# Kernel optimization log

Hardware: AMD Instinct MI355X
Metric: run time of the kernel (lower is better)

Reference implementation:

```python
import jax, jax.numpy as jnp
import numpy as np

B, H, HF = 2048, 128, 10  # batch, bi-LSTM hidden, fc-LSTM hidden


def _lstm(x_seq, h0, c0, Wih, Whh, bih, bhh):
    """Unidirectional LSTM, PyTorch gate order (i, f, g, o).
    x_seq: [T, B, I]. Returns final (h, c), each [B, H].
    Input projection is hoisted out of the scan (one big GEMM)."""
    pre = jnp.einsum('tbi,gi->tbg', x_seq, Wih) + bih + bhh  # [T, B, 4H]

    def step(carry, p):
        h, c = carry
        g = p + h @ Whh.T
        i, f, gg, o = jnp.split(g, 4, axis=-1)
        c = jax.nn.sigmoid(f) * c + jax.nn.sigmoid(i) * jnp.tanh(gg)
        h = jax.nn.sigmoid(o) * jnp.tanh(c)
        return (h, c), None

    (hT, cT), _ = jax.lax.scan(step, (h0, c0), pre)
    return hT, cT


def setup_inputs() -> dict:
    key = jax.random.key(0)
    ks = iter(jax.random.split(key, 40))
    s = 1.0 / np.sqrt(H)
    sf = 1.0 / np.sqrt(HF)
    u = lambda shape, sc: jax.random.uniform(next(ks), shape, jnp.float32, -sc, sc)
    inp = {"x": jax.random.normal(next(ks), (B, 28, 28), jnp.float32)}
    for name in ["lr_f", "lr_b", "ud_f", "ud_b"]:
        inp["Wih_" + name] = u((4 * H, 28), s)
        inp["Whh_" + name] = u((4 * H, H), s)
        inp["bih_" + name] = u((4 * H,), s)
        inp["bhh_" + name] = u((4 * H,), s)
    inp["Wih_fc"] = u((4 * HF, 1), sf)
    inp["Whh_fc"] = u((4 * HF, HF), sf)
    inp["bih_fc"] = u((4 * HF,), sf)
    inp["bhh_fc"] = u((4 * HF,), sf)
    for name in ["h0_lr", "c0_lr", "h0_ud", "c0_ud"]:
        inp[name] = jax.random.normal(next(ks), (2, B, H), jnp.float32)
    inp["h0_fc"] = jax.random.normal(next(ks), (B, HF), jnp.float32)
    inp["c0_fc"] = jax.random.normal(next(ks), (B, HF), jnp.float32)
    return inp


def reference(x, Wih_lr_f, Whh_lr_f, bih_lr_f, bhh_lr_f,
              Wih_lr_b, Whh_lr_b, bih_lr_b, bhh_lr_b,
              Wih_ud_f, Whh_ud_f, bih_ud_f, bhh_ud_f,
              Wih_ud_b, Whh_ud_b, bih_ud_b, bhh_ud_b,
              Wih_fc, Whh_fc, bih_fc, bhh_fc,
              h0_lr, c0_lr, h0_ud, c0_ud, h0_fc, c0_fc):
    x_lr = jnp.transpose(x, (1, 0, 2))  # [28, B, 28]: rows as time
    x_ud = jnp.transpose(x, (2, 0, 1))  # [28, B, 28]: cols as time
    # bidirectional = forward scan + scan over reversed sequence
    h_lr_f, _ = _lstm(x_lr, h0_lr[0], c0_lr[0], Wih_lr_f, Whh_lr_f, bih_lr_f, bhh_lr_f)
    h_lr_b, _ = _lstm(x_lr[::-1], h0_lr[1], c0_lr[1], Wih_lr_b, Whh_lr_b, bih_lr_b, bhh_lr_b)
    h_ud_f, _ = _lstm(x_ud, h0_ud[0], c0_ud[0], Wih_ud_f, Whh_ud_f, bih_ud_f, bhh_ud_f)
    h_ud_b, _ = _lstm(x_ud[::-1], h0_ud[1], c0_ud[1], Wih_ud_b, Whh_ud_b, bih_ud_b, bhh_ud_b)
    feat = jnp.concatenate([h_lr_f, h_lr_b, h_ud_f, h_ud_b], axis=1)  # [B, 4H]
    seq = feat.T[:, :, None]  # [4H, B, 1]: feature index is the fc-LSTM time axis
    h_f, _ = _lstm(seq, h0_fc, c0_fc, Wih_fc, Whh_fc, bih_fc, bhh_fc)  # [B, 10]
    return jax.nn.log_softmax(h_f, axis=1)
```

## Files before the change

kernel.cpp:

```cpp
#include <hip/hip_runtime.h>
#include <hip/hip_bf16.h>

typedef __bf16   bf16x8 __attribute__((ext_vector_type(8)));
typedef float    f32x4  __attribute__((ext_vector_type(4)));
typedef _Float16 h16x2  __attribute__((ext_vector_type(2)));

#define LOG2E 1.4426950408889634f
#define LN2   0.6931471805599453f

__device__ __forceinline__ float rcp_(float x){
#if __has_builtin(__builtin_amdgcn_rcpf)
  return __builtin_amdgcn_rcpf(x);
#else
  return 1.0f / x;
#endif
}
__device__ __forceinline__ float ex2_(float x){
#if __has_builtin(__builtin_amdgcn_exp2f)
  return __builtin_amdgcn_exp2f(x);
#else
  return exp2f(x);
#endif
}
__device__ __forceinline__ float lg2_(float x){
#if __has_builtin(__builtin_amdgcn_logf)
  return __builtin_amdgcn_logf(x);
#else
  return log2f(x);
#endif
}

__device__ __forceinline__ int pkrtz_(float a, float b){
  auto v = __builtin_amdgcn_cvt_pkrtz(a, b);
  int r; __builtin_memcpy(&r, &v, 4); return r;
}
__device__ __forceinline__ h16x2 as_h2_(int x){
  h16x2 r; __builtin_memcpy(&r, &x, 4); return r;
}

#if __has_builtin(__builtin_amdgcn_fdot2)
__device__ __forceinline__ float fdot2_(int w, int h, float a){
  return __builtin_amdgcn_fdot2(as_h2_(w), as_h2_(h), a, false);
}
#else
__device__ __forceinline__ float fdot2_(int w, int h, float a){
  h16x2 wv = as_h2_(w), hv = as_h2_(h);
  return a + (float)wv[0]*(float)hv[0] + (float)wv[1]*(float)hv[1];
}
#endif

struct LstmArgs {
  const float* Wih[4]; const float* Whh[4];
  const float* bih[4]; const float* bhh[4];
  const float* h0[4];  const float* c0[4];
};

__global__ void pack_weights(LstmArgs args, bf16x8* __restrict__ wpack,
                             float* __restrict__ bpack)
{
  const int idx = blockIdx.x*256 + threadIdx.x;
  if (idx >= 4*8*4*5*64) return;
  const int lane = idx & 63;
  int r = idx >> 6;
  const int kk = r % 5; r /= 5;
  const int g  = r & 3; r >>= 2;
  const int w  = r & 7;
  const int d  = r >> 3;
  const int lc = lane & 15, lr4 = lane >> 4;
  const int grow = g*128 + w*16 + lc;
  const float sc = (g == 2) ? 2.0f*LOG2E : -LOG2E;

  bf16x8 v;
  if (kk < 4){
    const float* p = args.Whh[d] + grow*128 + kk*32 + lr4*8;
#pragma unroll
    for (int j = 0; j < 8; ++j) v[j] = (__bf16)(p[j] * sc);
  } else {
#pragma unroll
    for (int j = 0; j < 8; ++j){
      const int xi = lr4*8 + j;
      v[j] = (xi < 28) ? (__bf16)(args.Wih[d][grow*28 + xi] * sc) : (__bf16)0.0f;
    }
  }
  wpack[idx] = v;
  if (kk == 0 && lr4 == 0)
    bpack[d*512 + grow] = (args.bih[d][grow] + args.bhh[d][grow]) * sc;
}

__global__ __launch_bounds__(512, 2) void lstm4_kernel(const float* __restrict__ x,
                                                       LstmArgs args,
                                                       const bf16x8* __restrict__ wpack,
                                                       const float* __restrict__ bpack,
                                                       __bf16* __restrict__ featB)
{
  const int dir = blockIdx.x >> 6;
  const int b0  = (blockIdx.x & 63) * 32;
  const int tid = threadIdx.x;
  const int w   = tid >> 6;
  const int l   = tid & 63;
  const int lc  = l & 15;
  const int lr4 = l >> 4;

  const float* __restrict__ h0 = args.h0[dir];
  const float* __restrict__ c0 = args.c0[dir];
  const int rev = dir & 1;
  const bool lrdir = (dir < 2);

  __shared__ __align__(16) __bf16 hcat[2][32 * 168];
  __shared__ __align__(16) __bf16 xstage[28 * 32 * 40];

  bf16x8 bfr[4][5];
  f32x4  bias_acc[4];
  {
    const bf16x8* wp = wpack + (dir*8 + w)*4*5*64;
#pragma unroll
    for (int g = 0; g < 4; ++g){
#pragma unroll
      for (int kk = 0; kk < 5; ++kk)
        bfr[g][kk] = wp[(g*5 + kk)*64 + l];
      const float b = bpack[dir*512 + g*128 + w*16 + lc];
      f32x4 bv = {b, b, b, b};
      bias_acc[g] = bv;
    }
  }

  for (int idx = tid; idx < 32*196; idx += 512){
    const int row = idx / 196;
    const int rem = idx - row*196;
    if (lrdir){
      const int t = rem / 7, jg = rem - 7*t;
      const float4 v = *(const float4*)&x[(b0+row)*784 + t*28 + jg*4];
      __bf16* dst = &xstage[(t*32 + row)*40 + jg*4];
      dst[0]=(__bf16)v.x; dst[1]=(__bf16)v.y; dst[2]=(__bf16)v.z; dst[3]=(__bf16)v.w;
    } else {
      const int j = rem / 7, tg = rem - 7*j;
      const float4 v = *(const float4*)&x[(b0+row)*784 + j*28 + tg*4];
      xstage[((tg*4+0)*32 + row)*40 + j] = (__bf16)v.x;
      xstage[((tg*4+1)*32 + row)*40 + j] = (__bf16)v.y;
      xstage[((tg*4+2)*32 + row)*40 + j] = (__bf16)v.z;
      xstage[((tg*4+3)*32 + row)*40 + j] = (__bf16)v.w;
    }
  }
  for (int idx = tid; idx < 28*32; idx += 512){
    const int t = idx >> 5, row = idx & 31;
    __bf16* p = &xstage[(t*32 + row)*40 + 28];
    p[0] = p[1] = p[2] = p[3] = (__bf16)0.0f;
  }

  float cst[2][4];
#pragma unroll
  for (int m = 0; m < 2; ++m)
#pragma unroll
  for (int r = 0; r < 4; ++r){
    const int row = 16*m + 4*lr4 + r;
    const int col = w*16 + lc;
    cst[m][r] = c0[(b0+row)*128 + col];
    hcat[0][row*168 + col] = (__bf16)h0[(b0+row)*128 + col];
  }
  __syncthreads();

  int cur = 0;
  for (int s = 0; s < 28; ++s){
    const int t = rev ? (27 - s) : s;
    const int nxt = cur ^ 1;

    f32x4 acc[2][4];
#pragma unroll
    for (int m = 0; m < 2; ++m){
#pragma unroll
      for (int kk = 0; kk < 5; ++kk){
        const bf16x8 a = (kk < 4)
          ? *(const bf16x8*)&hcat[cur][(16*m + lc)*168 + kk*32 + lr4*8]
          : *(const bf16x8*)&xstage[(t*32 + 16*m + lc)*40 + lr4*8];
        if (kk == 0){
#pragma unroll
          for (int g = 0; g < 4; ++g)
            acc[m][g] = __builtin_amdgcn_mfma_f32_16x16x32_bf16(a, bfr[g][0], bias_acc[g], 0, 0, 0);
        } else {
#pragma unroll
          for (int g = 0; g < 4; ++g)
            acc[m][g] = __builtin_amdgcn_mfma_f32_16x16x32_bf16(a, bfr[g][kk], acc[m][g], 0, 0, 0);
        }
      }
    }

#pragma unroll
    for (int m = 0; m < 2; ++m)
#pragma unroll
    for (int r = 0; r < 4; ++r){
      const float Ei = ex2_(acc[m][0][r]);
      const float Ef = ex2_(acc[m][1][r]);
      const float Eg = ex2_(acc[m][2][r]);
      const float Eo = ex2_(acc[m][3][r]);
      const float u  = 1.0f + Ei;
      const float v  = 1.0f + Eg;
      const float wf = 1.0f + Ef;
      const float P  = u * v;
      const float R  = rcp_(P * wf);
      const float num = __builtin_fmaf(cst[m][r], P, (v - 2.0f) * wf);
      const float cc  = num * R;
      cst[m][r] = cc;
      const float Ec  = ex2_(2.0f*LOG2E*cc);
      const float roc = rcp_((1.0f + Eo)*(1.0f + Ec));
      const float hv  = (Ec - 1.0f)*roc;
      hcat[nxt][(16*m + 4*lr4 + r)*168 + w*16 + lc] = (__bf16)hv;
    }
    __syncthreads();
    cur = nxt;
  }

  {
    const int row = tid >> 4;
    const int cg  = tid & 15;
    const bf16x8 hv = *(const bf16x8*)&hcat[cur][row*168 + cg*8];
    *(bf16x8*)&featB[(b0+row)*512 + dir*128 + cg*8] = hv;
  }
}

__global__ __launch_bounds__(256) void fc_lstm_wave(const ushort* __restrict__ featB,
                                                    const float* __restrict__ Wih,
                                                    const float* __restrict__ Whh,
                                                    const float* __restrict__ bih,
                                                    const float* __restrict__ bhh,
                                                    const float* __restrict__ h0,
                                                    const float* __restrict__ c0,
                                                    float* __restrict__ out)
{
  const int tid = threadIdx.x;
  const int l   = tid & 63;
  const int e   = blockIdx.x*4 + (tid >> 6);
  const int u   = l >> 2;
  const int g   = l & 3;
  const int uc  = (u < 10) ? u : 9;
  const bool valid = (u < 10);
  const float sc = (g == 2) ? 2.0f*LOG2E : -LOG2E;
  const int row = g*10 + uc;

  int wh2[5];
#pragma unroll
  for (int m = 0; m < 5; ++m){
    const float w0 = valid ? Whh[row*10 + 2*m]   * sc : 0.0f;
    const float w1 = valid ? Whh[row*10 + 2*m+1] * sc : 0.0f;
    wh2[m] = pkrtz_(w0, w1);
  }
  const float wx   = valid ? Wih[row]*sc : 0.0f;
  const float bia  = valid ? (bih[row] + bhh[row])*sc : 0.0f;
  const float actA = (g == 2) ? 1.0f : 0.0f;
  const float actB = (g == 2) ? -2.0f : 1.0f;

  float c     = valid ? c0[e*10 + uc] : 0.0f;
  float hlast = valid ? h0[e*10 + uc] : 0.0f;

  int hp0, hp1, hp2, hp3, hp4;
  {
    const int hn = __builtin_amdgcn_mov_dpp(__float_as_int(hlast), 0x104, 0xF, 0xF, false);
    const int hpi = pkrtz_(hlast, __int_as_float(hn));
    hp0 = __builtin_amdgcn_readlane(hpi,  0);
    hp1 = __builtin_amdgcn_readlane(hpi,  8);
    hp2 = __builtin_amdgcn_readlane(hpi, 16);
    hp3 = __builtin_amdgcn_readlane(hpi, 24);
    hp4 = __builtin_amdgcn_readlane(hpi, 32);
  }

  const uint4* fBs;
  {
    unsigned long long a = (unsigned long long)(uintptr_t)(featB + (size_t)e*512);
    unsigned lo = (unsigned)__builtin_amdgcn_readfirstlane((int)(a & 0xffffffffu));
    unsigned hi = (unsigned)__builtin_amdgcn_readfirstlane((int)(a >> 32));
    fBs = (const uint4*)(uintptr_t)(((unsigned long long)hi << 32) | lo);
  }

  unsigned int cur[8][4], nxt[8][4];
#pragma unroll
  for (int k = 0; k < 8; ++k){
    const uint4 q0 = fBs[k];
    cur[k][0]=q0.x; cur[k][1]=q0.y; cur[k][2]=q0.z; cur[k][3]=q0.w;
    const uint4 q1 = fBs[8 + k];
    nxt[k][0]=q1.x; nxt[k][1]=q1.y; nxt[k][2]=q1.z; nxt[k][3]=q1.w;
  }

  for (int win = 0; win < 8; ++win){
#pragma unroll
    for (int blk = 0; blk < 8; ++blk){
#pragma unroll
      for (int jj = 0; jj < 8; ++jj){
        const unsigned d  = cur[blk][jj >> 1];
        const unsigned xb = (jj & 1) ? (d & 0xffff0000u) : (d << 16);
        const float xs = __int_as_float((int)xb);
        float a0 = __builtin_fmaf(wx, xs, bia);
        a0 = fdot2_(wh2[0], hp0, a0);
        float a1 = fdot2_(wh2[1], hp1, 0.0f);
        a0 = fdot2_(wh2[2], hp2, a0);
        a1 = fdot2_(wh2[3], hp3, a1);
        a0 = fdot2_(wh2[4], hp4, a0);
        const float acc = a0 + a1;
        const float rc  = rcp_(1.0f + ex2_(acc));
        const float val = __builtin_fmaf(actB, rc, actA);
        const int   vi  = __float_as_int(val);
        const float tg  = __int_as_float(__builtin_amdgcn_mov_dpp(vi, 0xAA, 0xF, 0xF, false));
        const float sf  = __int_as_float(__builtin_amdgcn_mov_dpp(vi, 0x55, 0xF, 0xF, false));
        const float so  = __int_as_float(__builtin_amdgcn_mov_dpp(vi, 0xFF, 0xF, 0xF, false));
        c = __builtin_fmaf(sf, c, val*tg);
        const float tc = __builtin_fmaf(-2.0f, rcp_(1.0f + ex2_(2.0f*LOG2E*c)), 1.0f);
        const float h  = so*tc;
        hlast = h;
        const int hn  = __builtin_amdgcn_mov_dpp(__float_as_int(h), 0x104, 0xF, 0xF, false);
        const int hpi = pkrtz_(h, __int_as_float(hn));
        hp0 = __builtin_amdgcn_readlane(hpi,  0);
        hp1 = __builtin_amdgcn_readlane(hpi,  8);
        hp2 = __builtin_amdgcn_readlane(hpi, 16);
        hp3 = __builtin_amdgcn_readlane(hpi, 24);
        hp4 = __builtin_amdgcn_readlane(hpi, 32);
      }
    }
#pragma unroll
    for (int k = 0; k < 8; ++k){
      cur[k][0]=nxt[k][0]; cur[k][1]=nxt[k][1];
      cur[k][2]=nxt[k][2]; cur[k][3]=nxt[k][3];
    }
    if (win < 6){
#pragma unroll
      for (int k = 0; k < 8; ++k){
        const uint4 q = fBs[(win + 2)*8 + k];
        nxt[k][0]=q.x; nxt[k][1]=q.y; nxt[k][2]=q.z; nxt[k][3]=q.w;
      }
    }
  }

  const int hb = __float_as_int(hlast);
  float sh[10];
#pragma unroll
  for (int m = 0; m < 10; ++m)
    sh[m] = __int_as_float(__builtin_amdgcn_readlane(hb, 4*m));
  float mx = sh[0];
#pragma unroll
  for (int m = 1; m < 10; ++m) mx = fmaxf(mx, sh[m]);
  float es = 0.0f;
#pragma unroll
  for (int m = 0; m < 10; ++m) es += ex2_(LOG2E*(sh[m] - mx));
  const float lse = LN2 * lg2_(es);
  if (valid && g == 0) out[e*10 + u] = hlast - mx - lse;
}

extern "C" void kernel_launch(void* const* d_in, const int* in_sizes, int n_in,
                              void* d_out, int out_size, void* d_ws, size_t ws_size,
                              hipStream_t stream)
{
  const float* x = (const float*)d_in[0];
  LstmArgs a;
  const int base[4] = {1, 5, 9, 13};
  for (int d = 0; d < 4; ++d){
    a.Wih[d] = (const float*)d_in[base[d] + 0];
    a.Whh[d] = (const float*)d_in[base[d] + 1];
    a.bih[d] = (const float*)d_in[base[d] + 2];
    a.bhh[d] = (const float*)d_in[base[d] + 3];
  }
  const float* h0lr = (const float*)d_in[21];
  const float* c0lr = (const float*)d_in[22];
  const float* h0ud = (const float*)d_in[23];
  const float* c0ud = (const float*)d_in[24];
  a.h0[0] = h0lr;               a.c0[0] = c0lr;
  a.h0[1] = h0lr + 2048*128;    a.c0[1] = c0lr + 2048*128;
  a.h0[2] = h0ud;               a.c0[2] = c0ud;
  a.h0[3] = h0ud + 2048*128;    a.c0[3] = c0ud + 2048*128;

  char* ws = (char*)d_ws;
  __bf16* featB = (__bf16*)ws;
  bf16x8* wpack = (bf16x8*)(ws + (2u<<20));
  float*  bpack = (float*)(ws + (2u<<20) + 655360u);

  pack_weights<<<160, 256, 0, stream>>>(a, wpack, bpack);
  lstm4_kernel<<<256, 512, 0, stream>>>(x, a, wpack, bpack, featB);
  fc_lstm_wave<<<512, 256, 0, stream>>>((const ushort*)featB,
      (const float*)d_in[17], (const float*)d_in[18],
      (const float*)d_in[19], (const float*)d_in[20],
      (const float*)d_in[25], (const float*)d_in[26],
      (float*)d_out);
}
```

Measured before the change: 126.4 us.

## Halve batch tile per LSTM block and fold bias into input MFMA column

Each block of the bidirectional LSTM kernel now handles 16 batch rows instead of 32, which doubles the grid to 512 blocks and raises the launch-bounds occupancy hint to 4 blocks per CU. The gate bias is folded into the padded input weight column, multiplied by a constant 1.0 written into the staged input. This removes the separate bias buffer and the bias accumulator registers. The aim is more parallelism across CUs on the latency-bound 28-step recurrence. In exchange each wave issues half as many MFMAs per step, and the bias is now rounded to bf16.

```diff
diff --git a/kernel.cpp b/kernel.cpp
--- a/kernel.cpp
+++ b/kernel.cpp
@@ -55,8 +55,7 @@
   const float* h0[4];  const float* c0[4];
 };
 
-__global__ void pack_weights(LstmArgs args, bf16x8* __restrict__ wpack,
-                             float* __restrict__ bpack)
+__global__ void pack_weights(LstmArgs args, bf16x8* __restrict__ wpack)
 {
   const int idx = blockIdx.x*256 + threadIdx.x;
   if (idx >= 4*8*4*5*64) return;
@@ -79,22 +78,23 @@
 #pragma unroll
     for (int j = 0; j < 8; ++j){
       const int xi = lr4*8 + j;
-      v[j] = (xi < 28) ? (__bf16)(args.Wih[d][grow*28 + xi] * sc) : (__bf16)0.0f;
+      float wv;
+      if (xi < 28)       wv = args.Wih[d][grow*28 + xi] * sc;
+      else if (xi == 28) wv = (args.bih[d][grow] + args.bhh[d][grow]) * sc;
+      else               wv = 0.0f;
+      v[j] = (__bf16)wv;
     }
   }
   wpack[idx] = v;
-  if (kk == 0 && lr4 == 0)
-    bpack[d*512 + grow] = (args.bih[d][grow] + args.bhh[d][grow]) * sc;
-}
-
-__global__ __launch_bounds__(512, 2) void lstm4_kernel(const float* __restrict__ x,
+}
+
+__global__ __launch_bounds__(512, 4) void lstm4_kernel(const float* __restrict__ x,
                                                        LstmArgs args,
                                                        const bf16x8* __restrict__ wpack,
-                                                       const float* __restrict__ bpack,
                                                        __bf16* __restrict__ featB)
 {
-  const int dir = blockIdx.x >> 6;
-  const int b0  = (blockIdx.x & 63) * 32;
+  const int dir = blockIdx.x >> 7;
+  const int b0  = (blockIdx.x & 127) * 16;
   const int tid = threadIdx.x;
   const int w   = tid >> 6;
   const int l   = tid & 63;
@@ -106,110 +106,100 @@
   const int rev = dir & 1;
   const bool lrdir = (dir < 2);
 
-  __shared__ __align__(16) __bf16 hcat[2][32 * 168];
-  __shared__ __align__(16) __bf16 xstage[28 * 32 * 40];
+  __shared__ __align__(16) __bf16 hcat[2][16 * 168];
+  __shared__ __align__(16) __bf16 xstage[28 * 16 * 40];
 
   bf16x8 bfr[4][5];
-  f32x4  bias_acc[4];
   {
     const bf16x8* wp = wpack + (dir*8 + w)*4*5*64;
 #pragma unroll
-    for (int g = 0; g < 4; ++g){
+    for (int g = 0; g < 4; ++g)
 #pragma unroll
       for (int kk = 0; kk < 5; ++kk)
         bfr[g][kk] = wp[(g*5 + kk)*64 + l];
-      const float b = bpack[dir*512 + g*128 + w*16 + lc];
-      f32x4 bv = {b, b, b, b};
-      bias_acc[g] = bv;
-    }
-  }
-
-  for (int idx = tid; idx < 32*196; idx += 512){
+  }
+
+  for (int idx = tid; idx < 16*196; idx += 512){
     const int row = idx / 196;
     const int rem = idx - row*196;
     if (lrdir){
       const int t = rem / 7, jg = rem - 7*t;
       const float4 v = *(const float4*)&x[(b0+row)*784 + t*28 + jg*4];
-      __bf16* dst = &xstage[(t*32 + row)*40 + jg*4];
+      __bf16* dst = &xstage[(t*16 + row)*40 + jg*4];
       dst[0]=(__bf16)v.x; dst[1]=(__bf16)v.y; dst[2]=(__bf16)v.z; dst[3]=(__bf16)v.w;
     } else {
       const int j = rem / 7, tg = rem - 7*j;
       const float4 v = *(const float4*)&x[(b0+row)*784 + j*28 + tg*4];
-      xstage[((tg*4+0)*32 + row)*40 + j] = (__bf16)v.x;
-      xstage[((tg*4+1)*32 + row)*40 + j] = (__bf16)v.y;
-      xstage[((tg*4+2)*32 + row)*40 + j] = (__bf16)v.z;
-      xstage[((tg*4+3)*32 + row)*40 + j] = (__bf16)v.w;
-    }
-  }
-  for (int idx = tid; idx < 28*32; idx += 512){
-    const int t = idx >> 5, row = idx & 31;
-    __bf16* p = &xstage[(t*32 + row)*40 + 28];
-    p[0] = p[1] = p[2] = p[3] = (__bf16)0.0f;
-  }
-
-  float cst[2][4];
-#pragma unroll
-  for (int m = 0; m < 2; ++m)
+      xstage[((tg*4+0)*16 + row)*40 + j] = (__bf16)v.x;
+      xstage[((tg*4+1)*16 + row)*40 + j] = (__bf16)v.y;
+      xstage[((tg*4+2)*16 + row)*40 + j] = (__bf16)v.z;
+      xstage[((tg*4+3)*16 + row)*40 + j] = (__bf16)v.w;
+    }
+  }
+  if (tid < 28*16){
+    const int t = tid >> 4, row = tid & 15;
+    __bf16* p = &xstage[(t*16 + row)*40 + 28];
+    p[0] = (__bf16)1.0f; p[1] = (__bf16)0.0f; p[2] = (__bf16)0.0f; p[3] = (__bf16)0.0f;
+  }
+
+  float cst[4];
 #pragma unroll
   for (int r = 0; r < 4; ++r){
-    const int row = 16*m + 4*lr4 + r;
+    const int row = 4*lr4 + r;
     const int col = w*16 + lc;
-    cst[m][r] = c0[(b0+row)*128 + col];
+    cst[r] = c0[(b0+row)*128 + col];
     hcat[0][row*168 + col] = (__bf16)h0[(b0+row)*128 + col];
   }
   __syncthreads();
+
+  const f32x4 zacc = {0.0f, 0.0f, 0.0f, 0.0f};
 
   int cur = 0;
   for (int s = 0; s < 28; ++s){
     const int t = rev ? (27 - s) : s;
     const int nxt = cur ^ 1;
 
-    f32x4 acc[2][4];
-#pragma unroll
-    for (int m = 0; m < 2; ++m){
-#pragma unroll
-      for (int kk = 0; kk < 5; ++kk){
-        const bf16x8 a = (kk < 4)
-          ? *(const bf16x8*)&hcat[cur][(16*m + lc)*168 + kk*32 + lr4*8]
-          : *(const bf16x8*)&xstage[(t*32 + 16*m + lc)*40 + lr4*8];
-        if (kk == 0){
-#pragma unroll
-          for (int g = 0; g < 4; ++g)
-            acc[m][g] = __builtin_amdgcn_mfma_f32_16x16x32_bf16(a, bfr[g][0], bias_acc[g], 0, 0, 0);
-        } else {
-#pragma unroll
-          for (int g = 0; g < 4; ++g)
-            acc[m][g] = __builtin_amdgcn_mfma_f32_16x16x32_bf16(a, bfr[g][kk], acc[m][g], 0, 0, 0);
-        }
+    f32x4 acc[4];
+#pragma unroll
+    for (int kk = 0; kk < 5; ++kk){
+      const bf16x8 a = (kk < 4)
+        ? *(const bf16x8*)&hcat[cur][lc*168 + kk*32 + lr4*8]
+        : *(const bf16x8*)&xstage[(t*16 + lc)*40 + lr4*8];
+      if (kk == 0){
+#pragma unroll
+        for (int g = 0; g < 4; ++g)
+          acc[g] = __builtin_amdgcn_mfma_f32_16x16x32_bf16(a, bfr[g][0], zacc, 0, 0, 0);
+      } else {
+#pragma unroll
+        for (int g = 0; g < 4; ++g)
+          acc[g] = __builtin_amdgcn_mfma_f32_16x16x32_bf16(a, bfr[g][kk], acc[g], 0, 0, 0);
       }
     }
 
 #pragma unroll
-    for (int m = 0; m < 2; ++m)
-#pragma unroll
     for (int r = 0; r < 4; ++r){
-      const float Ei = ex2_(acc[m][0][r]);
-      const float Ef = ex2_(acc[m][1][r]);
-      const float Eg = ex2_(acc[m][2][r]);
-      const float Eo = ex2_(acc[m][3][r]);
+      const float Ei = ex2_(acc[0][r]);
+      const float Ef = ex2_(acc[1][r]);
+      const float Eg = ex2_(acc[2][r]);
+      const float Eo = ex2_(acc[3][r]);
       const float u  = 1.0f + Ei;
       const float v  = 1.0f + Eg;
       const float wf = 1.0f + Ef;
       const float P  = u * v;
       const float R  = rcp_(P * wf);
-      const float num = __builtin_fmaf(cst[m][r], P, (v - 2.0f) * wf);
+      const float num = __builtin_fmaf(cst[r], P, (v - 2.0f) * wf);
       const float cc  = num * R;
-      cst[m][r] = cc;
+      cst[r] = cc;
       const float Ec  = ex2_(2.0f*LOG2E*cc);
       const float roc = rcp_((1.0f + Eo)*(1.0f + Ec));
       const float hv  = (Ec - 1.0f)*roc;
-      hcat[nxt][(16*m + 4*lr4 + r)*168 + w*16 + lc] = (__bf16)hv;
+      hcat[nxt][(4*lr4 + r)*168 + w*16 + lc] = (__bf16)hv;
     }
     __syncthreads();
     cur = nxt;
   }
 
-  {
+  if (tid < 256){
     const int row = tid >> 4;
     const int cg  = tid & 15;
     const bf16x8 hv = *(const bf16x8*)&hcat[cur][row*168 + cg*8];
@@ -367,10 +357,9 @@
   char* ws = (char*)d_ws;
   __bf16* featB = (__bf16*)ws;
   bf16x8* wpack = (bf16x8*)(ws + (2u<<20));
-  float*  bpack = (float*)(ws + (2u<<20) + 655360u);
-
-  pack_weights<<<160, 256, 0, stream>>>(a, wpack, bpack);
-  lstm4_kernel<<<256, 512, 0, stream>>>(x, a, wpack, bpack, featB);
+
+  pack_weights<<<160, 256, 0, stream>>>(a, wpack);
+  lstm4_kernel<<<512, 512, 0, stream>>>(x, a, wpack, featB);
   fc_lstm_wave<<<512, 256, 0, stream>>>((const ushort*)featB,
       (const float*)d_in[17], (const float*)d_in[18],
       (const float*)d_in[19], (const float*)d_in[20],
```

New measurement: 122.3 us. -3.3%, faster.
